# Kernel tuning notes

Hardware: AMD Instinct MI355X
Metric: run time of the kernel (lower is better)

Reference implementation:

```python
import jax, jax.numpy as jnp
import numpy as np

NEG = jnp.float32(-1e9)
N_PRE = 12000   # n_train_pre_nms (module default training=True)
N_POST = 2000   # n_train_post_nms
MIN_SIZE = 16.0
NMS_THRESH = 0.7


def _make_anchors(feat_size=64, stride=16):
    scales = np.array([128.0, 256.0, 512.0])
    ratios = np.array([0.5, 1.0, 2.0])
    ws = (scales[:, None] * np.sqrt(1.0 / ratios)[None, :]).reshape(-1)  # [9]
    hs = (scales[:, None] * np.sqrt(ratios)[None, :]).reshape(-1)        # [9]
    ctr = (np.arange(feat_size) + 0.5) * stride
    cy, cx = np.meshgrid(ctr, ctr, indexing='ij')
    cx = cx.reshape(-1, 1); cy = cy.reshape(-1, 1)                       # [4096,1]
    x1 = cx - 0.5 * ws[None, :]; y1 = cy - 0.5 * hs[None, :]
    x2 = cx + 0.5 * ws[None, :]; y2 = cy + 0.5 * hs[None, :]
    return np.stack([x1, y1, x2, y2], axis=-1).reshape(-1, 4).astype(np.float32)  # [36864,4]


def setup_inputs() -> dict:
    key = jax.random.key(0)
    k1, k2 = jax.random.split(key)
    anchors = jnp.asarray(_make_anchors())[None]            # [1, 36864, 4]
    B, N = 8, anchors.shape[1]
    pred_loc = jax.random.normal(k1, (B, N, 4), jnp.float32) * 0.2
    pred_obj = jax.random.normal(k2, (B, N, 2), jnp.float32)
    return {"img_height": 1024, "img_width": 1024,
            "anchor_boxes": anchors, "pred_loc": pred_loc, "pred_obj": pred_obj}


def _decode(anchors, loc, img_w, img_h):
    # anchors [N,4] (x1,y1,x2,y2), loc [N,4] (dx,dy,dw,dh)
    w = anchors[:, 2] - anchors[:, 0]
    h = anchors[:, 3] - anchors[:, 1]
    cx = anchors[:, 0] + 0.5 * w
    cy = anchors[:, 1] + 0.5 * h
    pcx = loc[:, 0] * w + cx
    pcy = loc[:, 1] * h + cy
    pw = jnp.exp(loc[:, 2]) * w
    ph = jnp.exp(loc[:, 3]) * h
    x1 = jnp.clip(pcx - 0.5 * pw, 0.0, img_w)
    y1 = jnp.clip(pcy - 0.5 * ph, 0.0, img_h)
    x2 = jnp.clip(pcx + 0.5 * pw, 0.0, img_w)
    y2 = jnp.clip(pcy + 0.5 * ph, 0.0, img_h)
    return jnp.stack([x1, y1, x2, y2], axis=-1)  # [N,4]


def _iou_one_vs_all(box, boxes):
    # box [4], boxes [M,4]
    ix1 = jnp.maximum(box[0], boxes[:, 0])
    iy1 = jnp.maximum(box[1], boxes[:, 1])
    ix2 = jnp.minimum(box[2], boxes[:, 2])
    iy2 = jnp.minimum(box[3], boxes[:, 3])
    inter = jnp.maximum(ix2 - ix1, 0.0) * jnp.maximum(iy2 - iy1, 0.0)
    a0 = (box[2] - box[0]) * (box[3] - box[1])
    a1 = (boxes[:, 2] - boxes[:, 0]) * (boxes[:, 3] - boxes[:, 1])
    return inter / jnp.maximum(a0 + a1 - inter, 1e-9)


def _greedy_nms(boxes, scores):
    # boxes [M,4], scores [M] (invalid entries already NEG). Selects the first
    # N_POST boxes kept by greedy IoU suppression (exactly torchvision nms +
    # [:n_post] truncation, since greedy NMS emits in descending-score order).
    def step(s, _):
        i = jnp.argmax(s)
        valid = s[i] > NEG * 0.5
        box = boxes[i]
        suppress = _iou_one_vs_all(box, boxes) > NMS_THRESH  # includes self
        s = jnp.where(suppress, NEG, s)
        return s, (box, valid)
    _, (kept, mask) = jax.lax.scan(step, scores, None, length=N_POST)
    return jnp.where(mask[:, None], kept, 0.0), mask  # [N_POST,4], [N_POST]


def reference(img_height, img_width, anchor_boxes, pred_loc, pred_obj):
    img_h = jnp.float32(img_height)
    img_w = jnp.float32(img_width)
    anchors = anchor_boxes[0]                                    # [N,4]
    scores = jax.nn.softmax(pred_obj, axis=2)[:, :, 1]           # [B,N]
    boxes = jax.vmap(lambda l: _decode(anchors, l, img_w, img_h))(pred_loc)  # [B,N,4]
    # min-size filter -> mask scores instead of dynamic filtering
    valid = jnp.all(boxes[..., 2:] - boxes[..., :2] >= MIN_SIZE, axis=-1)    # [B,N]
    scores = jnp.where(valid, scores, NEG)
    # descending sort + pre-NMS truncation == top_k
    top_s, top_i = jax.lax.top_k(scores, N_PRE)                  # [B,N_PRE]
    top_boxes = jnp.take_along_axis(boxes, top_i[..., None], axis=1)         # [B,N_PRE,4]
    kept_boxes, kept_mask = jax.vmap(_greedy_nms)(top_boxes, top_s)
    return kept_boxes, kept_mask  # [B,N_POST,4] padded, [B,N_POST] validity
```

## Files before the change

### kernel.cpp

```cpp
#include <hip/hip_runtime.h>

typedef unsigned long long u64;
typedef unsigned int u32;

#define B_SZ   8
#define N_ANC  36864
#define N_PRE  12000
#define N_POST 2000
#define SEG    2048
#define NSEG   6
#define MAXC   (SEG * NSEG)
#define NW     (SEG / 64)
#define NDW    (MAXC / 64)
#define NBLK   144

__device__ __forceinline__ float area_of(float4 p) {
  return __fmul_rn(__fsub_rn(p.z, p.x), __fsub_rn(p.w, p.y));
}

__device__ __forceinline__ bool iou_gt_a(float4 p, float4 q, float a0, float a1) {
  float ix1 = fmaxf(p.x, q.x), iy1 = fmaxf(p.y, q.y);
  float ix2 = fminf(p.z, q.z), iy2 = fminf(p.w, q.w);
  float iw = fmaxf(__fsub_rn(ix2, ix1), 0.0f);
  float ih = fmaxf(__fsub_rn(iy2, iy1), 0.0f);
  float inter = __fmul_rn(iw, ih);
  float den = fmaxf(__fsub_rn(__fadd_rn(a0, a1), inter), 1e-9f);
  return (inter / den) > 0.7f;
}

__global__ __launch_bounds__(256) void k_decode(
    const int* __restrict__ imh_p, const int* __restrict__ imw_p,
    const float* __restrict__ anchors, const float* __restrict__ loc,
    const float* __restrict__ obj, float4* __restrict__ boxes,
    u64* __restrict__ keys, u32* __restrict__ hist)
{
  __shared__ u32 lh[2048];
  int t = threadIdx.x;
#pragma unroll
  for (int i = 0; i < 8; ++i) lh[t + i * 256] = 0;
  __syncthreads();

  int n = blockIdx.x * 256 + t;
  int b = blockIdx.y;
  float a0 = anchors[n * 4 + 0], a1 = anchors[n * 4 + 1];
  float a2 = anchors[n * 4 + 2], a3 = anchors[n * 4 + 3];
  size_t off = (size_t)b * N_ANC + n;
  float l0 = loc[off * 4 + 0], l1 = loc[off * 4 + 1];
  float l2 = loc[off * 4 + 2], l3 = loc[off * 4 + 3];

  float w  = __fsub_rn(a2, a0);
  float h  = __fsub_rn(a3, a1);
  float cx = __fadd_rn(a0, __fmul_rn(0.5f, w));
  float cy = __fadd_rn(a1, __fmul_rn(0.5f, h));
  float pcx = __fadd_rn(__fmul_rn(l0, w), cx);
  float pcy = __fadd_rn(__fmul_rn(l1, h), cy);
  float pw  = __fmul_rn(expf(l2), w);
  float ph  = __fmul_rn(expf(l3), h);
  float imw = (float)imw_p[0], imh = (float)imh_p[0];
  float hx = __fmul_rn(0.5f, pw), hy = __fmul_rn(0.5f, ph);
  float x1 = fminf(fmaxf(__fsub_rn(pcx, hx), 0.0f), imw);
  float y1 = fminf(fmaxf(__fsub_rn(pcy, hy), 0.0f), imh);
  float x2 = fminf(fmaxf(__fadd_rn(pcx, hx), 0.0f), imw);
  float y2 = fminf(fmaxf(__fadd_rn(pcy, hy), 0.0f), imh);
  boxes[off] = make_float4(x1, y1, x2, y2);

  bool valid = (__fsub_rn(x2, x1) >= 16.0f) && (__fsub_rn(y2, y1) >= 16.0f);

  float o0 = obj[off * 2 + 0], o1 = obj[off * 2 + 1];
  float m  = fmaxf(o0, o1);
  float e0 = expf(__fsub_rn(o0, m));
  float e1 = expf(__fsub_rn(o1, m));
  float s  = e1 / __fadd_rn(e0, e1);
  float sc = valid ? s : -1e9f;

  u32 u  = __float_as_uint(sc);
  u32 fk = (u & 0x80000000u) ? ~u : (u | 0x80000000u);
  u32 sk = ~fk;
  u64 key = ((u64)sk << 32) | (u32)n;
  keys[off] = key;
  atomicAdd(&lh[(u32)(key >> 53)], 1u);
  __syncthreads();
#pragma unroll
  for (int i = 0; i < 8; ++i) {
    u32 v = lh[t + i * 256];
    if (v) atomicAdd(&hist[b * 2048 + t + i * 256], v);
  }
}

__global__ __launch_bounds__(256) void k_pick1(
    const u32* __restrict__ hist, u32* __restrict__ T1, u32* __restrict__ Base1)
{
  int b = blockIdx.x, t = threadIdx.x;
  const u32* h = hist + b * 2048;
  __shared__ u32 part[256], pre[256];
  u32 loc[8], s = 0;
#pragma unroll
  for (int i = 0; i < 8; ++i) { loc[i] = h[t * 8 + i]; s += loc[i]; }
  part[t] = s;
  __syncthreads();
  if (t == 0) { u32 acc = 0; for (int i = 0; i < 256; ++i) { pre[i] = acc; acc += part[i]; } }
  __syncthreads();
  u32 acc = pre[t];
#pragma unroll
  for (int i = 0; i < 8; ++i) {
    u32 na = acc + loc[i];
    if (acc < N_PRE && na >= N_PRE) { T1[b] = (u32)(t * 8 + i); Base1[b] = acc; }
    acc = na;
  }
}

__global__ __launch_bounds__(256) void k_hist2(
    const u64* __restrict__ keys, const u32* __restrict__ T1,
    u32* __restrict__ hist)
{
  int b = blockIdx.y;
  u32 t1 = T1[b];
  __shared__ u32 lh[2048];
  int t = threadIdx.x;
#pragma unroll
  for (int i = 0; i < 8; ++i) lh[t + i * 256] = 0;
  __syncthreads();
#pragma unroll
  for (int k = 0; k < 4; ++k) {
    int i = blockIdx.x * 1024 + k * 256 + t;
    u64 key = keys[(size_t)b * N_ANC + i];
    if ((u32)(key >> 53) == t1) atomicAdd(&lh[(u32)(key >> 42) & 0x7FFu], 1u);
  }
  __syncthreads();
#pragma unroll
  for (int i = 0; i < 8; ++i) {
    u32 v = lh[t + i * 256];
    if (v) atomicAdd(&hist[b * 2048 + t + i * 256], v);
  }
}

__global__ __launch_bounds__(256) void k_pick2(
    const u32* __restrict__ hist, const u32* __restrict__ T1,
    const u32* __restrict__ Base1, u32* __restrict__ T2)
{
  int b = blockIdx.x, t = threadIdx.x;
  const u32* h = hist + b * 2048;
  __shared__ u32 part[256], pre[256];
  u32 loc[8], s = 0;
#pragma unroll
  for (int i = 0; i < 8; ++i) { loc[i] = h[t * 8 + i]; s += loc[i]; }
  part[t] = s;
  __syncthreads();
  if (t == 0) { u32 acc = Base1[b]; for (int i = 0; i < 256; ++i) { pre[i] = acc; acc += part[i]; } }
  __syncthreads();
  u32 acc = pre[t];
#pragma unroll
  for (int i = 0; i < 8; ++i) {
    u32 na = acc + loc[i];
    if (acc < N_PRE && na >= N_PRE) T2[b] = (T1[b] << 11) | (u32)(t * 8 + i);
    acc = na;
  }
}

__global__ __launch_bounds__(256) void k_count(
    const u64* __restrict__ keys, const u32* __restrict__ T2,
    u32* __restrict__ bcnt)
{
  int b = blockIdx.y;
  int i = blockIdx.x * 256 + threadIdx.x;
  u64 key = keys[(size_t)b * N_ANC + i];
  bool pred = (u32)(key >> 42) <= T2[b];
  u64 bal = __ballot(pred);
  __shared__ u32 wc[4];
  int wv = threadIdx.x >> 6, lane = threadIdx.x & 63;
  if (lane == 0) wc[wv] = (u32)__popcll(bal);
  __syncthreads();
  if (threadIdx.x == 0)
    bcnt[b * NBLK + blockIdx.x] = wc[0] + wc[1] + wc[2] + wc[3];
}

__global__ __launch_bounds__(64) void k_scan(
    const u32* __restrict__ bcnt, u32* __restrict__ boff)
{
  int b = blockIdx.x;
  if (threadIdx.x == 0) {
    u32 acc = 0;
    for (int i = 0; i < NBLK; ++i) { boff[b * NBLK + i] = acc; acc += bcnt[b * NBLK + i]; }
  }
}

__global__ __launch_bounds__(256) void k_scatter(
    const u64* __restrict__ keys, const u32* __restrict__ T2,
    const u32* __restrict__ boff, u64* __restrict__ cand)
{
  int b = blockIdx.y;
  int i = blockIdx.x * 256 + threadIdx.x;
  u64 key = keys[(size_t)b * N_ANC + i];
  bool pred = (u32)(key >> 42) <= T2[b];
  u64 bal = __ballot(pred);
  __shared__ u32 wc[4];
  int wv = threadIdx.x >> 6, lane = threadIdx.x & 63;
  if (lane == 0) wc[wv] = (u32)__popcll(bal);
  __syncthreads();
  u32 base = boff[b * NBLK + blockIdx.x];
  for (int w = 0; w < wv; ++w) base += wc[w];
  u32 rank = (u32)__popcll(bal & ((1ull << lane) - 1ull));
  if (pred) {
    u32 pos = base + rank;
    if (pos < MAXC) cand[(size_t)b * MAXC + pos] = key;
  }
}

#define SIDX(x) ((x) + ((x) >> 5))
__global__ __launch_bounds__(1024) void k_sort_tile(u64* __restrict__ a)
{
  int b = blockIdx.y, base = blockIdx.x * 2048;
  u64* p = a + (size_t)b * MAXC + base;
  __shared__ u64 lds[2048 + 64];
  int t = threadIdx.x;
  lds[SIDX(t)] = p[t];
  lds[SIDX(t + 1024)] = p[t + 1024];
  __syncthreads();
  for (int k = 2; k <= 2048; k <<= 1) {
    for (int j = k >> 1; j > 0; j >>= 1) {
      int i = ((t & ~(j - 1)) << 1) | (t & (j - 1));
      int l = i | j;
      bool asc = ((i & k) == 0);
      u64 x = lds[SIDX(i)], y = lds[SIDX(l)];
      if ((x > y) == asc) { lds[SIDX(i)] = y; lds[SIDX(l)] = x; }
      __syncthreads();
    }
  }
  p[t] = lds[SIDX(t)];
  p[t + 1024] = lds[SIDX(t + 1024)];
}

__global__ __launch_bounds__(256) void k_merge_gather(
    const u64* __restrict__ cand, const float4* __restrict__ boxes,
    float4* __restrict__ gbox, u64* __restrict__ deadm)
{
  int b = blockIdx.y;
  int p = blockIdx.x * 256 + threadIdx.x;
  const u64* cb = cand + (size_t)b * MAXC;
  u64 key = cb[p];
  int r = p >> 11;
  int rank = p & 2047;
#pragma unroll
  for (int s = 0; s < NSEG; ++s) {
    if (s == r) continue;
    const u64* run = cb + (s << 11);
    int lo = 0;
#pragma unroll
    for (int step = 2048; step >= 1; step >>= 1) {
      int np = lo + step;
      if (np <= 2048 && run[np - 1] < key) lo = np;
    }
    rank += lo;
  }
  bool valid = ((u32)(key >> 32) < 0x80000000u) && (rank < N_PRE);
  float4 bx = make_float4(0.f, 0.f, 0.f, 0.f);
  if (valid) bx = boxes[(size_t)b * N_ANC + (u32)key];
  gbox[(size_t)b * MAXC + rank] = bx;
  if (!valid) atomicOr(&deadm[b * NDW + (rank >> 6)], 1ull << (rank & 63));
}

__device__ __forceinline__ void segmask_tile(
    int b, int sg, int tile, const float4* __restrict__ gbox,
    u64* __restrict__ smask, u64* __restrict__ smaskT,
    float4* rbox, float* rarea, u64* diag)
{
  int r = tile, rg = 0;
  while (r >= 32 - rg) { r -= 32 - rg; ++rg; }
  int cw = rg + r;
  const float4* gb = gbox + (size_t)b * MAXC + sg * SEG;
  int t = threadIdx.x;
  if (t < 64) { float4 bx = gb[rg * 64 + t]; rbox[t] = bx; rarea[t] = area_of(bx); }
  __syncthreads();
  int wv = t >> 6, lane = t & 63;
  u64* srow = smask + (size_t)(b * NSEG + sg) * SEG * NW + (size_t)rg * 64 * NW;
  float4 cb4 = gb[cw * 64 + lane];
  float ca = area_of(cb4);
  bool isdiag = (cw == rg);
  for (int rr = wv * 16; rr < wv * 16 + 16; ++rr) {
    bool p = iou_gt_a(rbox[rr], cb4, rarea[rr], ca);
    if (isdiag) p = p && (lane > rr);
    u64 m = __ballot(p);
    if (lane == 0) { srow[(size_t)rr * NW + cw] = m; if (isdiag) diag[rr] = m; }
  }
  if (isdiag) {
    __syncthreads();
    if (t < 64) {
      u64 s = 0;
      for (int q = 0; q < 64; ++q) s |= ((diag[q] >> t) & 1ull) << q;
      smaskT[(size_t)(b * NSEG + sg) * SEG + rg * 64 + t] = s;
    }
  }
}

__global__ __launch_bounds__(256) void k_segmask01(
    const float4* __restrict__ gbox, u64* __restrict__ smask,
    u64* __restrict__ smaskT)
{
  __shared__ float4 rbox[64]; __shared__ float rarea[64]; __shared__ u64 diag[64];
  int b = blockIdx.y;
  int sg = blockIdx.x / 528, tile = blockIdx.x % 528;
  segmask_tile(b, sg, tile, gbox, smask, smaskT, rbox, rarea, diag);
}

__device__ __forceinline__ void cross_work(
    int b, int sg, int bx, const float4* __restrict__ gbox,
    const float4* __restrict__ keptb, const int* __restrict__ meta,
    u64* __restrict__ deadm, float4* kb, float* ka)
{
  int kc = bx >> 3, cbk = bx & 7;
  int nkept = meta[b * 8 + 0];
  int kbase = kc * 256;
  if (kbase >= nkept) return;
  int kcnt = min(256, nkept - kbase);
  int t = threadIdx.x;
  if (t < kcnt) {
    float4 k4 = keptb[(size_t)b * SEG + kbase + t];
    kb[t] = k4; ka[t] = area_of(k4);
  }
  __syncthreads();
  int gi = sg * SEG + cbk * 256 + t;
  float4 my = gbox[(size_t)b * MAXC + gi];
  float ma = area_of(my);
  bool sup = false;
  for (int kk = 0; kk < kcnt; ++kk) {
    if (iou_gt_a(kb[kk], my, ka[kk], ma)) { sup = true; break; }
  }
  u64 bm = __ballot(sup);
  if ((t & 63) == 0 && bm) atomicOr(&deadm[b * NDW + (gi >> 6)], bm);
}

__global__ __launch_bounds__(256) void k_cross(
    const float4* __restrict__ gbox, const float4* __restrict__ keptb,
    const int* __restrict__ meta, u64* __restrict__ deadm, int sg)
{
  int b = blockIdx.y;
  if (meta[b * 8 + 1]) return;
  __shared__ float4 kb[256]; __shared__ float ka[256];
  cross_work(b, sg, blockIdx.x, gbox, keptb, meta, deadm, kb, ka);
}

__global__ __launch_bounds__(256) void k_crossmask(
    const float4* __restrict__ gbox, const float4* __restrict__ keptb,
    const int* __restrict__ meta, u64* __restrict__ deadm,
    u64* __restrict__ smask, u64* __restrict__ smaskT, int sg)
{
  int b = blockIdx.y;
  if (meta[b * 8 + 1]) return;
  __shared__ float4 kb[256]; __shared__ float ka[256]; __shared__ u64 diag[64];
  if (blockIdx.x < 64) {
    cross_work(b, sg, blockIdx.x, gbox, keptb, meta, deadm, kb, ka);
  } else {
    segmask_tile(b, sg, blockIdx.x - 64, gbox, smask, smaskT,
                 kb, ka, diag);
  }
}

__global__ __launch_bounds__(1024) void k_walk(
    const float4* __restrict__ gbox, const u64* __restrict__ smask,
    const u64* __restrict__ smaskT, const u64* __restrict__ deadm,
    int* __restrict__ meta, float4* __restrict__ keptb,
    float* __restrict__ out, int sg)
{
  int b = blockIdx.x;
  if (meta[b * 8 + 1]) return;
  int t = threadIdx.x, wv = t >> 6, lane = t & 63;

  __shared__ u64 rowbuf[2][2048];
  __shared__ u64 stbuf[2][64];
  __shared__ float4 bbox[2][64];
  __shared__ u64 sdead[2];
  __shared__ u32 remv[64];
  __shared__ u32 klist[64];
  __shared__ int s_stop, s_nkept, s_kcnt;

  const u64* smb = smask + (size_t)(b * NSEG + sg) * SEG * NW;
  const u64* stb = smaskT + (size_t)(b * NSEG + sg) * SEG;
  const u64* dmb = deadm + b * NDW + sg * NW;
  const float4* gb = gbox + (size_t)b * MAXC + sg * SEG;
  float4* kbuf = keptb + (size_t)b * SEG;
  float4* ob = (float4*)(out + (size_t)b * N_POST * 4);
  float* om = out + (size_t)B_SZ * N_POST * 4 + (size_t)b * N_POST;

  {
    u64 a = smb[t], c = smb[t + 1024];
    u64 st_ = 0; float4 bb_ = make_float4(0.f, 0.f, 0.f, 0.f);
    if (t < 64) { st_ = stb[t]; bb_ = gb[t]; }
    u64 sd_ = (t == 0) ? dmb[0] : 0;
    rowbuf[0][t] = a;
    rowbuf[0][t + 1024] = c;
    if (t < 64) { stbuf[0][t] = st_; bbox[0][t] = bb_; remv[t] = 0; }
    if (t == 0) { sdead[0] = sd_; s_stop = 0; s_nkept = meta[b * 8 + 0]; }
  }
  __syncthreads();

  int p0 = t - 64, p1 = p0 + 960, p2 = p0 + 1920;
  for (int g = 0; g < NW; ++g) {
    int cb = g & 1, nb = cb ^ 1;
    if (wv > 0) {
      if (g < NW - 1) {
        const u64* src = smb + (size_t)(g + 1) * 2048;
        u64 a  = src[p0];
        u64 c  = src[p1];
        u64 e  = (p0 < 128) ? src[p2] : 0;
        u64 st_ = 0; float4 bb_ = make_float4(0.f, 0.f, 0.f, 0.f);
        if (p0 < 64) { st_ = stb[(g + 1) * 64 + p0]; bb_ = gb[(g + 1) * 64 + p0]; }
        u64 sd_ = (t == 64) ? dmb[g + 1] : 0;
        rowbuf[nb][p0] = a;
        rowbuf[nb][p1] = c;
        if (p0 < 128) rowbuf[nb][p2] = e;
        if (p0 < 64) { stbuf[nb][p0] = st_; bbox[nb][p0] = bb_; }
        if (t == 64) sdead[nb] = sd_;
      }
    } else {
      int l = lane;
      u64 S = stbuf[cb][l];
      u64 remg = ((u64)remv[2 * g + 1] << 32) | remv[2 * g];
      u64 avail = ~(remg | sdead[cb]);
      u64 km = 0;
      while (avail) {
        bool al = (avail >> l) & 1;
        u64 newk = __ballot(al && (S & avail) == 0ull);
        u64 nd   = __ballot(al && (S & newk) != 0ull);
        km |= newk;
        avail &= ~(newk | nd);
      }
      int nk0 = s_nkept;
      int rem = N_POST - nk0;
      int kc = __popcll(km);
      bool stop = (kc >= rem);
      int rank = __popcll(km & ((1ull << l) - 1ull));
      if (((km >> l) & 1) && rank < rem) {
        float4 bx = bbox[cb][l];
        kbuf[nk0 + rank] = bx;
        ob[nk0 + rank] = bx;
        om[nk0 + rank] = 1.0f;
        klist[rank] = (u32)l;
      }
      if (l == 0) {
        int eff = stop ? rem : kc;
        s_kcnt = eff;
        s_nkept = nk0 + eff;
        if (stop) s_stop = 1;
      }
    }
    __syncthreads();
    if (s_stop) break;
    if (g < NW - 1) {
      int kcnt = s_kcnt;
      u32* rb32 = (u32*)rowbuf[cb];
      for (int i = t; i < kcnt * 64; i += 1024) {
        int kk = i >> 6, w = i & 63;
        if ((w >> 1) > g) {
          u32 v = rb32[klist[kk] * 64 + w];
          if (v) atomicOr(&remv[w], v);
        }
      }
    }
    __syncthreads();
  }
  int nk = s_nkept;
  bool fin = s_stop || (sg == NSEG - 1);
  if (t == 0) { meta[b * 8 + 0] = nk; if (fin) meta[b * 8 + 1] = 1; }
  if (fin) {
    float4 zero = make_float4(0.f, 0.f, 0.f, 0.f);
    for (int i = nk + t; i < N_POST; i += 1024) { ob[i] = zero; om[i] = 0.0f; }
  }
}

extern "C" void kernel_launch(void* const* d_in, const int* in_sizes, int n_in,
                              void* d_out, int out_size, void* d_ws, size_t ws_size,
                              hipStream_t stream)
{
  const int*   imh     = (const int*)d_in[0];
  const int*   imw     = (const int*)d_in[1];
  const float* anchors = (const float*)d_in[2];
  const float* loc     = (const float*)d_in[3];
  const float* obj     = (const float*)d_in[4];
  float* out = (float*)d_out;

  char* ws = (char*)d_ws;
  size_t off = 0;
  float4* boxes = (float4*)(ws + off); off += (size_t)B_SZ * N_ANC * 16;
  u64*    keys  = (u64*)   (ws + off); off += (size_t)B_SZ * N_ANC * 8;
  u64*    cand  = (u64*)   (ws + off); off += (size_t)B_SZ * MAXC * 8;
  float4* gbox  = (float4*)(ws + off); off += (size_t)B_SZ * MAXC * 16;
  float4* keptb = (float4*)(ws + off); off += (size_t)B_SZ * SEG * 16;
  off = (off + 255) & ~(size_t)255;
  char*   zr    = ws + off;
  u32*    hist1 = (u32*)(zr);
  u32*    hist2 = (u32*)(zr + 65536);
  u32*    T1    = (u32*)(zr + 131072);
  u32*    Base1 = (u32*)(zr + 131072 + 32);
  u32*    T2    = (u32*)(zr + 131072 + 64);
  int*    meta  = (int*)(zr + 131072 + 128);
  u64*    deadm = (u64*)(zr + 131072 + 128 + 256);
  u32*    bcnt  = (u32*)(zr + 131072 + 128 + 256 + (size_t)B_SZ * NDW * 8);
  u32*    boff  = bcnt + (size_t)B_SZ * NBLK;
  size_t  zr_sz = 131072 + 128 + 256 + (size_t)B_SZ * NDW * 8
                + 2 * (size_t)B_SZ * NBLK * 4;
  off += (zr_sz + 255) & ~(size_t)255;
  u64*    smask  = (u64*)(ws + off); off += (size_t)B_SZ * NSEG * SEG * NW * 8;
  u64*    smaskT = (u64*)(ws + off); off += (size_t)B_SZ * NSEG * SEG * 8;

  hipMemsetAsync(zr, 0, zr_sz, stream);
  hipMemsetAsync(cand, 0xFF, (size_t)B_SZ * MAXC * 8, stream);

  k_decode<<<dim3(NBLK, B_SZ), 256, 0, stream>>>(imh, imw, anchors, loc, obj,
                                                 boxes, keys, hist1);
  k_pick1<<<B_SZ, 256, 0, stream>>>(hist1, T1, Base1);
  k_hist2<<<dim3(36, B_SZ), 256, 0, stream>>>(keys, T1, hist2);
  k_pick2<<<B_SZ, 256, 0, stream>>>(hist2, T1, Base1, T2);

  k_count<<<dim3(NBLK, B_SZ), 256, 0, stream>>>(keys, T2, bcnt);
  k_scan<<<B_SZ, 64, 0, stream>>>(bcnt, boff);
  k_scatter<<<dim3(NBLK, B_SZ), 256, 0, stream>>>(keys, T2, boff, cand);

  k_sort_tile<<<dim3(NSEG, B_SZ), 1024, 0, stream>>>(cand);
  k_merge_gather<<<dim3(MAXC / 256, B_SZ), 256, 0, stream>>>(cand, boxes, gbox, deadm);

  k_segmask01<<<dim3(1056, B_SZ), 256, 0, stream>>>(gbox, smask, smaskT);

  k_walk<<<B_SZ, 1024, 0, stream>>>(gbox, smask, smaskT, deadm, meta, keptb, out, 0);
  k_cross<<<dim3(64, B_SZ), 256, 0, stream>>>(gbox, keptb, meta, deadm, 1);
  k_walk<<<B_SZ, 1024, 0, stream>>>(gbox, smask, smaskT, deadm, meta, keptb, out, 1);
  for (int sg = 2; sg < NSEG; ++sg) {
    k_crossmask<<<dim3(592, B_SZ), 256, 0, stream>>>(gbox, keptb, meta, deadm,
                                                     smask, smaskT, sg);
    k_walk<<<B_SZ, 1024, 0, stream>>>(gbox, smask, smaskT, deadm, meta, keptb, out, sg);
  }
}
```

Baseline: 222.6 us.

## Fold block-offset scan into scatter and prefetch walk rows two steps ahead

Removes the separate single-thread scan kernel: each scatter block now sums the preceding block counts from shared memory to get its base offset, saving one launch. In the serial walk kernel, the loader waves now issue global loads for group g+2 into registers while the current group is processed, so memory latency overlaps the walk and the prefetch buffer becomes a register stage. It also skips the suppression OR loop when no boxes were kept in a group. Trade-offs are more registers per thread and a redundant serial prefix sum in every scatter block.

```diff
diff --git a/kernel.cpp b/kernel.cpp
--- a/kernel.cpp
+++ b/kernel.cpp
@@ -174,30 +174,25 @@
     bcnt[b * NBLK + blockIdx.x] = wc[0] + wc[1] + wc[2] + wc[3];
 }
 
-__global__ __launch_bounds__(64) void k_scan(
-    const u32* __restrict__ bcnt, u32* __restrict__ boff)
-{
-  int b = blockIdx.x;
-  if (threadIdx.x == 0) {
-    u32 acc = 0;
-    for (int i = 0; i < NBLK; ++i) { boff[b * NBLK + i] = acc; acc += bcnt[b * NBLK + i]; }
-  }
-}
-
 __global__ __launch_bounds__(256) void k_scatter(
     const u64* __restrict__ keys, const u32* __restrict__ T2,
-    const u32* __restrict__ boff, u64* __restrict__ cand)
-{
-  int b = blockIdx.y;
-  int i = blockIdx.x * 256 + threadIdx.x;
-  u64 key = keys[(size_t)b * N_ANC + i];
+    const u32* __restrict__ bcnt, u64* __restrict__ cand)
+{
+  int b = blockIdx.y, bx = blockIdx.x;
+  int t = threadIdx.x;
+  __shared__ u32 cnts[NBLK];
+  __shared__ u32 wc[4];
+  __shared__ u32 sbase;
+  if (t < NBLK) cnts[t] = bcnt[b * NBLK + t];
+  u64 key = keys[(size_t)b * N_ANC + bx * 256 + t];
   bool pred = (u32)(key >> 42) <= T2[b];
   u64 bal = __ballot(pred);
-  __shared__ u32 wc[4];
-  int wv = threadIdx.x >> 6, lane = threadIdx.x & 63;
+  int wv = t >> 6, lane = t & 63;
   if (lane == 0) wc[wv] = (u32)__popcll(bal);
   __syncthreads();
-  u32 base = boff[b * NBLK + blockIdx.x];
+  if (t == 0) { u32 a = 0; for (int i = 0; i < bx; ++i) a += cnts[i]; sbase = a; }
+  __syncthreads();
+  u32 base = sbase;
   for (int w = 0; w < wv; ++w) base += wc[w];
   u32 rank = (u32)__popcll(bal & ((1ull << lane) - 1ull));
   if (pred) {
@@ -391,25 +386,36 @@
     if (t < 64) { stbuf[0][t] = st_; bbox[0][t] = bb_; remv[t] = 0; }
     if (t == 0) { sdead[0] = sd_; s_stop = 0; s_nkept = meta[b * 8 + 0]; }
   }
-  __syncthreads();
-
   int p0 = t - 64, p1 = p0 + 960, p2 = p0 + 1920;
+  u64 ra = 0, rc = 0, re = 0, rst = 0, rsd = 0;
+  float4 rbb = make_float4(0.f, 0.f, 0.f, 0.f);
+  if (wv > 0) {
+    const u64* src = smb + 2048;
+    ra = src[p0];
+    rc = src[p1];
+    if (p0 < 128) re = src[p2];
+    if (p0 < 64) { rst = stb[64 + p0]; rbb = gb[64 + p0]; }
+    if (t == 64) rsd = dmb[1];
+  }
+  __syncthreads();
+
   for (int g = 0; g < NW; ++g) {
     int cb = g & 1, nb = cb ^ 1;
     if (wv > 0) {
       if (g < NW - 1) {
-        const u64* src = smb + (size_t)(g + 1) * 2048;
-        u64 a  = src[p0];
-        u64 c  = src[p1];
-        u64 e  = (p0 < 128) ? src[p2] : 0;
-        u64 st_ = 0; float4 bb_ = make_float4(0.f, 0.f, 0.f, 0.f);
-        if (p0 < 64) { st_ = stb[(g + 1) * 64 + p0]; bb_ = gb[(g + 1) * 64 + p0]; }
-        u64 sd_ = (t == 64) ? dmb[g + 1] : 0;
-        rowbuf[nb][p0] = a;
-        rowbuf[nb][p1] = c;
-        if (p0 < 128) rowbuf[nb][p2] = e;
-        if (p0 < 64) { stbuf[nb][p0] = st_; bbox[nb][p0] = bb_; }
-        if (t == 64) sdead[nb] = sd_;
+        rowbuf[nb][p0] = ra;
+        rowbuf[nb][p1] = rc;
+        if (p0 < 128) rowbuf[nb][p2] = re;
+        if (p0 < 64) { stbuf[nb][p0] = rst; bbox[nb][p0] = rbb; }
+        if (t == 64) sdead[nb] = rsd;
+      }
+      if (g < NW - 2) {
+        const u64* src = smb + (size_t)(g + 2) * 2048;
+        ra = src[p0];
+        rc = src[p1];
+        if (p0 < 128) re = src[p2];
+        if (p0 < 64) { rst = stb[(g + 2) * 64 + p0]; rbb = gb[(g + 2) * 64 + p0]; }
+        if (t == 64) rsd = dmb[g + 2];
       }
     } else {
       int l = lane;
@@ -447,12 +453,14 @@
     if (s_stop) break;
     if (g < NW - 1) {
       int kcnt = s_kcnt;
-      u32* rb32 = (u32*)rowbuf[cb];
-      for (int i = t; i < kcnt * 64; i += 1024) {
-        int kk = i >> 6, w = i & 63;
-        if ((w >> 1) > g) {
-          u32 v = rb32[klist[kk] * 64 + w];
-          if (v) atomicOr(&remv[w], v);
+      if (kcnt) {
+        u32* rb32 = (u32*)rowbuf[cb];
+        for (int i = t; i < kcnt * 64; i += 1024) {
+          int kk = i >> 6, w = i & 63;
+          if ((w >> 1) > g) {
+            u32 v = rb32[klist[kk] * 64 + w];
+            if (v) atomicOr(&remv[w], v);
+          }
         }
       }
     }
@@ -495,9 +503,8 @@
   int*    meta  = (int*)(zr + 131072 + 128);
   u64*    deadm = (u64*)(zr + 131072 + 128 + 256);
   u32*    bcnt  = (u32*)(zr + 131072 + 128 + 256 + (size_t)B_SZ * NDW * 8);
-  u32*    boff  = bcnt + (size_t)B_SZ * NBLK;
   size_t  zr_sz = 131072 + 128 + 256 + (size_t)B_SZ * NDW * 8
-                + 2 * (size_t)B_SZ * NBLK * 4;
+                + (size_t)B_SZ * NBLK * 4;
   off += (zr_sz + 255) & ~(size_t)255;
   u64*    smask  = (u64*)(ws + off); off += (size_t)B_SZ * NSEG * SEG * NW * 8;
   u64*    smaskT = (u64*)(ws + off); off += (size_t)B_SZ * NSEG * SEG * 8;
@@ -512,8 +519,7 @@
   k_pick2<<<B_SZ, 256, 0, stream>>>(hist2, T1, Base1, T2);
 
   k_count<<<dim3(NBLK, B_SZ), 256, 0, stream>>>(keys, T2, bcnt);
-  k_scan<<<B_SZ, 64, 0, stream>>>(bcnt, boff);
-  k_scatter<<<dim3(NBLK, B_SZ), 256, 0, stream>>>(keys, T2, boff, cand);
+  k_scatter<<<dim3(NBLK, B_SZ), 256, 0, stream>>>(keys, T2, bcnt, cand);
 
   k_sort_tile<<<dim3(NSEG, B_SZ), 1024, 0, stream>>>(cand);
   k_merge_gather<<<dim3(MAXC / 256, B_SZ), 256, 0, stream>>>(cand, boxes, gbox, deadm);
```

After: 216.1 us (median of 2 runs). 1.03x faster.
